# Performance work log

Hardware: AMD Instinct MI355X
Metric: run time of the kernel (lower is better)

The kernel has to match this reference:

```python
import jax, jax.numpy as jnp
import numpy as np

N = 50000       # nodes
F_IN = 256
F_OUT = 64
H = 4           # heads
DEG = 16        # avg degree (random edges per node)
NEG_SLOPE = 0.2


def setup_inputs() -> dict:
    key = jax.random.key(0)
    k_h, k_e, k_w, k_fc = jax.random.split(key, 4)
    h = jax.random.normal(k_h, (N, F_IN), dtype=jnp.float32)
    # random edges + explicit self-loops so every node has >= 1 out-edge
    e_rand = jax.random.randint(k_e, (2, N * DEG), 0, N, dtype=jnp.int64)
    loops = jnp.tile(jnp.arange(N, dtype=jnp.int64)[None, :], (2, 1))
    edge_index = jnp.concatenate([e_rand, loops], axis=1)  # [2, 850000]
    # Glorot-uniform-like scales
    s_w = np.sqrt(6.0 / (F_IN + F_OUT)).astype(np.float32)
    s_a = np.sqrt(6.0 / (2 * F_OUT + 1)).astype(np.float32)
    w = jax.random.uniform(k_w, (H, F_IN, F_OUT), jnp.float32, -s_w, s_w)
    fc = jax.random.uniform(k_fc, (H, 2 * F_OUT, 1), jnp.float32, -s_a, s_a)
    bias = jnp.zeros((F_OUT,), jnp.float32)
    return {"h": h, "edge_index": edge_index, "w": w, "fc": fc, "bias": bias}


def reference(h, edge_index, w, fc, bias):
    # GAT forward, vectorized over edges (dropout is identity at inference).
    n = h.shape[0]
    f_out = w.shape[2]
    src, dst = edge_index[0], edge_index[1]           # [E]
    h_prime = jnp.einsum('nf,hfo->hno', h, w)          # [H, N, F]
    a = fc[..., 0]                                     # [H, 2F]
    a_src, a_dst = a[:, :f_out], a[:, f_out:]          # [H, F] each
    s_src = jnp.einsum('hnf,hf->hn', h_prime, a_src)   # [H, N] score of center node
    s_dst = jnp.einsum('hnf,hf->hn', h_prime, a_dst)   # [H, N] score of neighbor
    e = jax.nn.leaky_relu(s_src[:, src] + s_dst[:, dst], NEG_SLOPE)  # [H, E]
    e = e.T                                            # [E, H]
    # segment softmax over edges grouped by source node
    seg_max = jax.ops.segment_max(e, src, num_segments=n)   # [N, H]
    ex = jnp.exp(e - seg_max[src])                           # [E, H]
    denom = jax.ops.segment_sum(ex, src, num_segments=n)    # [N, H]
    alpha = ex / denom[src]                                  # [E, H]
    # scatter-aggregate: out_i = sum_{j in N(i)} alpha_ij * Wh_j
    msgs = alpha[:, :, None] * jnp.transpose(h_prime[:, dst, :], (1, 0, 2))  # [E, H, F]
    out = jax.ops.segment_sum(msgs, src, num_segments=n)    # [N, H, F]
    return out.mean(axis=1) + bias                           # [N, F]
```

## Files before the change

### kernel.cpp

```cpp
#include <hip/hip_runtime.h>
#include <cfloat>

#define FIN 256
#define FOUT 64
#define NH 4
#define NEG_SLOPE 0.2f
#define SLOTS 64
#define BCAP 3072
#define P1T 4096

typedef __bf16 bf16x8 __attribute__((ext_vector_type(8)));
typedef float f32x4 __attribute__((ext_vector_type(4)));

__device__ __forceinline__ ushort f2bf(float f) {
    return (ushort)((__float_as_uint(f) + 0x8000u) >> 16);
}
__device__ __forceinline__ float bf2f(ushort u) {
    return __uint_as_float(((unsigned)u) << 16);
}
__device__ __forceinline__ float lrelu(float x) {
    return (x >= 0.f) ? x : NEG_SLOPE * x;
}

__global__ __launch_bounds__(256) void k0_wconv(const float* __restrict__ w,
                                                ushort* __restrict__ wt,
                                                int* __restrict__ gcur, int gn)
{
    if ((int)blockIdx.x < 256) {
        const int g = blockIdx.x * 256 + threadIdx.x;
        const int hh  = g >> 14;
        const int rem = g & 16383;
        const int c   = rem >> 8;
        const int k   = rem & 255;
        wt[g] = f2bf(w[(((hh << 8) | k) << 6) | c]);
    } else {
        const int g = ((int)blockIdx.x - 256) * 256 + threadIdx.x;
        if (g < gn) gcur[g] = 0;
    }
}

__global__ __launch_bounds__(256) void k1a(
    const int* __restrict__ ei, int E, int nbuck,
    int* __restrict__ gcur, unsigned* __restrict__ barea)
{
    __shared__ int lcnt[512];
    __shared__ int lscan[512];
    __shared__ int lbase[512];
    __shared__ unsigned ledges[P1T];
    const int tid = threadIdx.x;

    for (int b = tid; b < 512; b += 256) lcnt[b] = 0;
    __syncthreads();

    const int e0 = (int)blockIdx.x * P1T;
    const int cnt_total = min(P1T, E - e0);
    int s[16], d[16];
#pragma unroll
    for (int i = 0; i < 16; ++i) {
        const int e = e0 + i * 256 + tid;
        if (e < E) {
            s[i] = ei[e];
            d[i] = ei[E + e];
            atomicAdd(&lcnt[s[i] >> 7], 1);
        } else {
            s[i] = -1; d[i] = 0;
        }
    }
    __syncthreads();

    if (tid < 64) {
        int vals[8], sum = 0;
#pragma unroll
        for (int k = 0; k < 8; ++k) { vals[k] = lcnt[tid * 8 + k]; sum += vals[k]; }
        int x = sum;
#pragma unroll
        for (int dd = 1; dd < 64; dd <<= 1) {
            const int t = __shfl_up(x, dd);
            if (tid >= dd) x += t;
        }
        int run = x - sum;
#pragma unroll
        for (int k = 0; k < 8; ++k) { lscan[tid * 8 + k] = run; run += vals[k]; }
    }
    __syncthreads();

    for (int b = tid; b < nbuck; b += 256) {
        const int c = lcnt[b];
        lbase[b] = c ? atomicAdd(&gcur[b * 16], c) : 0;
    }
    __syncthreads();
    for (int b = tid; b < 512; b += 256) lcnt[b] = 0;
    __syncthreads();

#pragma unroll
    for (int i = 0; i < 16; ++i) {
        if (s[i] >= 0) {
            const int b = s[i] >> 7;
            const int r = atomicAdd(&lcnt[b], 1);
            ledges[lscan[b] + r] =
                ((unsigned)b << 23) | ((unsigned)(s[i] & 127) << 16) |
                (unsigned)d[i];
        }
    }
    __syncthreads();

    for (int j = tid; j < cnt_total; j += 256) {
        const unsigned p = ledges[j];
        const int b = (int)(p >> 23);
        const int pos = lbase[b] + (j - lscan[b]);
        if (pos < BCAP)
            barea[(size_t)b * BCAP + pos] = p & 0x007FFFFFu;
    }
}

#define ASTRIDE 280
#define OSTRIDE 260
__global__ __launch_bounds__(512) void k_gemm(
    const float* __restrict__ h, const ushort* __restrict__ wt,
    const float* __restrict__ fc, ushort* __restrict__ hp,
    float* __restrict__ s_src, float* __restrict__ s_dst, int N)
{
    __shared__ ushort lds[64 * ASTRIDE];
    const int tid = threadIdx.x;
    const int n0 = (int)blockIdx.x * 64;

    {
        float4 va[8];
#pragma unroll
        for (int i = 0; i < 8; ++i) {
            const int idx = i * 512 + tid;
            const int row  = idx >> 6;
            const int quad = idx & 63;
            const int n = n0 + row;
            va[i] = (n < N) ? ((const float4*)(h + (size_t)n * FIN))[quad]
                            : make_float4(0.f, 0.f, 0.f, 0.f);
        }
#pragma unroll
        for (int i = 0; i < 8; ++i) {
            const int idx = i * 512 + tid;
            const int row  = idx >> 6;
            const int quad = idx & 63;
            ushort4 bv;
            bv.x = f2bf(va[i].x); bv.y = f2bf(va[i].y);
            bv.z = f2bf(va[i].z); bv.w = f2bf(va[i].w);
            *(ushort4*)&lds[row * ASTRIDE + quad * 4] = bv;
        }
    }
    __syncthreads();

    const int wid   = tid >> 6;
    const int head  = wid & 3;
    const int mhalf = wid >> 2;
    const int lane  = tid & 63;
    const int lrow  = lane & 15;
    const int lq    = lane >> 4;

    const ushort* wth = wt + head * (64 * 256);

    f32x4 acc[2][4];
#pragma unroll
    for (int mt = 0; mt < 2; ++mt)
#pragma unroll
        for (int nt = 0; nt < 4; ++nt)
            acc[mt][nt] = (f32x4){0.f, 0.f, 0.f, 0.f};

#pragma unroll
    for (int kt = 0; kt < 8; ++kt) {
        const int kof = kt * 32 + lq * 8;
        bf16x8 bfr[4];
#pragma unroll
        for (int nt = 0; nt < 4; ++nt)
            bfr[nt] = *(const bf16x8*)&wth[(nt * 16 + lrow) * 256 + kof];
        bf16x8 af[2];
#pragma unroll
        for (int mt = 0; mt < 2; ++mt)
            af[mt] = *(const bf16x8*)
                &lds[(mhalf * 32 + mt * 16 + lrow) * ASTRIDE + kof];
#pragma unroll
        for (int nt = 0; nt < 4; ++nt)
#pragma unroll
            for (int mt = 0; mt < 2; ++mt)
                acc[mt][nt] = __builtin_amdgcn_mfma_f32_16x16x32_bf16(
                    af[mt], bfr[nt], acc[mt][nt], 0, 0, 0);
    }

    float as_[4], ad_[4];
#pragma unroll
    for (int nt = 0; nt < 4; ++nt) {
        as_[nt] = fc[head * 2 * FOUT + nt * 16 + lrow];
        ad_[nt] = fc[head * 2 * FOUT + FOUT + nt * 16 + lrow];
    }
#pragma unroll
    for (int mt = 0; mt < 2; ++mt) {
        const int rbase = n0 + mhalf * 32 + mt * 16 + lq * 4;
#pragma unroll
        for (int r = 0; r < 4; ++r) {
            const int n = rbase + r;
            float ps = 0.f, pd = 0.f;
#pragma unroll
            for (int nt = 0; nt < 4; ++nt) {
                const float v = acc[mt][nt][r];
                ps = fmaf(v, as_[nt], ps);
                pd = fmaf(v, ad_[nt], pd);
            }
            ps += __shfl_xor(ps, 1); pd += __shfl_xor(pd, 1);
            ps += __shfl_xor(ps, 2); pd += __shfl_xor(pd, 2);
            ps += __shfl_xor(ps, 4); pd += __shfl_xor(pd, 4);
            ps += __shfl_xor(ps, 8); pd += __shfl_xor(pd, 8);
            if (lrow == 0 && n < N) {
                s_src[(size_t)n * NH + head] = ps;
                s_dst[(size_t)n * NH + head] = pd;
            }
        }
    }

    __syncthreads();
#pragma unroll
    for (int mt = 0; mt < 2; ++mt)
#pragma unroll
        for (int r = 0; r < 4; ++r)
#pragma unroll
            for (int nt = 0; nt < 4; ++nt)
                lds[(mhalf * 32 + mt * 16 + lq * 4 + r) * OSTRIDE +
                    (nt * 16 + lrow) * 4 + head] = f2bf(acc[mt][nt][r]);
    __syncthreads();
    for (int idx = tid; idx < 64 * 64; idx += 512) {
        const int row = idx >> 6;
        const int c   = idx & 63;
        const int n = n0 + row;
        if (n < N)
            *(ushort4*)&hp[(size_t)n * 256 + c * 4] =
                *(const ushort4*)&lds[row * OSTRIDE + c * 4];
    }
}

__global__ __launch_bounds__(256) void k2(
    const int* __restrict__ gcur, const unsigned* __restrict__ barea,
    ushort* __restrict__ col, int* __restrict__ cursor)
{
    __shared__ ushort colT[128 * SLOTS];
    __shared__ int cnt[128];
    const int tid = threadIdx.x;
    const int b = blockIdx.x;
    for (int i = tid; i < 128; i += 256) cnt[i] = 0;
    __syncthreads();
    int c = gcur[b * 16];
    if (c > BCAP) c = BCAP;
    for (int j = tid; j < c; j += 256) {
        const unsigned p = barea[(size_t)b * BCAP + j];
        const int sl = (int)((p >> 16) & 127);
        const int r = atomicAdd(&cnt[sl], 1);
        if (r < SLOTS) colT[sl * SLOTS + r] = (ushort)(p & 0xFFFFu);
    }
    __syncthreads();
    const size_t gbase = (size_t)b * 128 * SLOTS;
    for (int idx = tid; idx < 128 * SLOTS / 4; idx += 256)
        *(ushort4*)&col[gbase + (size_t)idx * 4] =
            *(const ushort4*)&colT[idx * 4];
    for (int i = tid; i < 128; i += 256)
        cursor[b * 128 + i] = cnt[i];
}

__global__ __launch_bounds__(256) void k_agg(
    const int* __restrict__ cursor, const ushort* __restrict__ col,
    const ushort* __restrict__ hp,
    const float* __restrict__ s_src, const float* __restrict__ s_dst,
    const float* __restrict__ bias, float* __restrict__ out, int N)
{
    const int wid  = threadIdx.x >> 6;
    const int lane = threadIdx.x & 63;
    const int n    = blockIdx.x * 4 + wid;
    if (n >= N) return;

    const size_t start = (size_t)n * SLOTS;
    const int deg = min(cursor[n], SLOTS);
    const float4 ssn = ((const float4*)s_src)[n];
    const float4* sd4 = (const float4*)s_dst;

    float4 acc = make_float4(0.f, 0.f, 0.f, 0.f);

    int dreg = 0;
    float4 x = make_float4(-FLT_MAX, -FLT_MAX, -FLT_MAX, -FLT_MAX);
    if (lane < deg) {
        dreg = col[start + lane];
        const float4 sd = sd4[dreg];
        x.x = lrelu(ssn.x + sd.x);
        x.y = lrelu(ssn.y + sd.y);
        x.z = lrelu(ssn.z + sd.z);
        x.w = lrelu(ssn.w + sd.w);
    }
    float4 m = x;
#pragma unroll
    for (int d = 32; d; d >>= 1) {
        m.x = fmaxf(m.x, __shfl_xor(m.x, d));
        m.y = fmaxf(m.y, __shfl_xor(m.y, d));
        m.z = fmaxf(m.z, __shfl_xor(m.z, d));
        m.w = fmaxf(m.w, __shfl_xor(m.w, d));
    }
    float4 e = make_float4(0.f, 0.f, 0.f, 0.f);
    if (lane < deg) {
        e.x = __expf(x.x - m.x);
        e.y = __expf(x.y - m.y);
        e.z = __expf(x.z - m.z);
        e.w = __expf(x.w - m.w);
    }
    float4 s = e;
#pragma unroll
    for (int d = 32; d; d >>= 1) {
        s.x += __shfl_xor(s.x, d);
        s.y += __shfl_xor(s.y, d);
        s.z += __shfl_xor(s.z, d);
        s.w += __shfl_xor(s.w, d);
    }
    float4 alpha;
    alpha.x = e.x / s.x;
    alpha.y = e.y / s.y;
    alpha.z = e.z / s.z;
    alpha.w = e.w / s.w;

    const int nblk = (deg + 3) >> 2;
    for (int b = 0; b < nblk; ++b) {
        int dd[4]; float4 av[4]; ushort4 v[4];
#pragma unroll
        for (int u = 0; u < 4; ++u) {
            const int j = b * 4 + u;
            dd[u]   = __shfl(dreg, j);
            av[u].x = __shfl(alpha.x, j);
            av[u].y = __shfl(alpha.y, j);
            av[u].z = __shfl(alpha.z, j);
            av[u].w = __shfl(alpha.w, j);
        }
#pragma unroll
        for (int u = 0; u < 4; ++u)
            v[u] = *(const ushort4*)&hp[((size_t)dd[u] * FOUT + lane) * NH];
#pragma unroll
        for (int u = 0; u < 4; ++u) {
            acc.x = fmaf(av[u].x, bf2f(v[u].x), acc.x);
            acc.y = fmaf(av[u].y, bf2f(v[u].y), acc.y);
            acc.z = fmaf(av[u].z, bf2f(v[u].z), acc.z);
            acc.w = fmaf(av[u].w, bf2f(v[u].w), acc.w);
        }
    }

    out[(size_t)n * FOUT + lane] =
        (acc.x + acc.y + acc.z + acc.w) * 0.25f + bias[lane];
}

extern "C" void kernel_launch(void* const* d_in, const int* in_sizes, int n_in,
                              void* d_out, int out_size, void* d_ws, size_t ws_size,
                              hipStream_t stream)
{
    const float* h    = (const float*)d_in[0];
    const int*   ei   = (const int*)d_in[1];
    const float* w    = (const float*)d_in[2];
    const float* fc   = (const float*)d_in[3];
    const float* bias = (const float*)d_in[4];
    float* out = (float*)d_out;

    const int N = in_sizes[0] / FIN;
    const int E = in_sizes[1] / 2;
    const int nbuck = (N + 127) >> 7;

    char* ws = (char*)d_ws;
    auto take = [&](size_t bytes) {
        char* p = ws;
        ws += (bytes + 255) & ~(size_t)255;
        return p;
    };
    ushort*   wt      = (ushort*)take((size_t)NH * FIN * FOUT * sizeof(ushort));
    ushort*   h_prime = (ushort*)take((size_t)NH * N * FOUT * sizeof(ushort));
    float*    s_src   = (float*)take((size_t)NH * N * sizeof(float));
    float*    s_dst   = (float*)take((size_t)NH * N * sizeof(float));
    int*      cursor  = (int*)take((size_t)nbuck * 128 * sizeof(int));
    ushort*   col     = (ushort*)take((size_t)nbuck * 128 * SLOTS * sizeof(ushort));
    int*      gcur    = (int*)take((size_t)nbuck * 16 * sizeof(int));
    unsigned* barea   = (unsigned*)take((size_t)nbuck * BCAP * sizeof(unsigned));

    const int gn = nbuck * 16;
    k0_wconv<<<256 + (gn + 255) / 256, 256, 0, stream>>>(w, wt, gcur, gn);

    const int p1B = (E + P1T - 1) / P1T;
    k1a<<<p1B, 256, 0, stream>>>(ei, E, nbuck, gcur, barea);

    k_gemm<<<(N + 63) / 64, 512, 0, stream>>>(h, wt, fc, h_prime,
                                              s_src, s_dst, N);

    k2<<<nbuck, 256, 0, stream>>>(gcur, barea, col, cursor);

    k_agg<<<(N + 3) / 4, 256, 0, stream>>>(cursor, col, h_prime,
                                           s_src, s_dst, bias, out, N);
}
```

Measured before the change: 151.6 us.

## Pre-convert h to bf16 in edge-bucketing kernel and split aggregation launch

The fp32-to-bf16 conversion of h moves out of the GEMM and into extra blocks of the edge-bucketing kernel, so the GEMM loads half the bytes per tile and skips the conversion step. The aim is to overlap the memory-bound conversion with the edge-partitioning work. This adds a full extra read of h in fp32 plus a bf16 write and reread through a new workspace buffer. The aggregation kernel is also split into three launches over node ranges, which adds launch overhead with no clear benefit on a single stream.

```diff
diff --git a/kernel.cpp b/kernel.cpp
--- a/kernel.cpp
+++ b/kernel.cpp
@@ -11,6 +11,7 @@
 
 typedef __bf16 bf16x8 __attribute__((ext_vector_type(8)));
 typedef float f32x4 __attribute__((ext_vector_type(4)));
+typedef unsigned short ushort8 __attribute__((ext_vector_type(8)));
 
 __device__ __forceinline__ ushort f2bf(float f) {
     return (ushort)((__float_as_uint(f) + 0x8000u) >> 16);
@@ -39,15 +40,35 @@
     }
 }
 
-__global__ __launch_bounds__(256) void k1a(
+__global__ __launch_bounds__(256) void k_prep(
     const int* __restrict__ ei, int E, int nbuck,
-    int* __restrict__ gcur, unsigned* __restrict__ barea)
+    int* __restrict__ gcur, unsigned* __restrict__ barea, int p1B,
+    const float* __restrict__ h, ushort* __restrict__ hbf, int hElems)
 {
     __shared__ int lcnt[512];
     __shared__ int lscan[512];
     __shared__ int lbase[512];
     __shared__ unsigned ledges[P1T];
     const int tid = threadIdx.x;
+
+    if ((int)blockIdx.x >= p1B) {
+        const int t = ((int)blockIdx.x - p1B) * 256 + tid;
+        const size_t base = (size_t)t * 16;
+        if (base + 16 <= (size_t)hElems) {
+            const float4* h4 = (const float4*)(h + base);
+            const float4 a0 = h4[0], a1 = h4[1], a2 = h4[2], a3 = h4[3];
+            ushort8 b0, b1;
+            b0[0]=f2bf(a0.x); b0[1]=f2bf(a0.y); b0[2]=f2bf(a0.z); b0[3]=f2bf(a0.w);
+            b0[4]=f2bf(a1.x); b0[5]=f2bf(a1.y); b0[6]=f2bf(a1.z); b0[7]=f2bf(a1.w);
+            b1[0]=f2bf(a2.x); b1[1]=f2bf(a2.y); b1[2]=f2bf(a2.z); b1[3]=f2bf(a2.w);
+            b1[4]=f2bf(a3.x); b1[5]=f2bf(a3.y); b1[6]=f2bf(a3.z); b1[7]=f2bf(a3.w);
+            *(ushort8*)&hbf[base]     = b0;
+            *(ushort8*)&hbf[base + 8] = b1;
+        } else {
+            for (size_t i = base; i < (size_t)hElems; ++i) hbf[i] = f2bf(h[i]);
+        }
+        return;
+    }
 
     for (int b = tid; b < 512; b += 256) lcnt[b] = 0;
     __syncthreads();
@@ -115,8 +136,8 @@
 
 #define ASTRIDE 280
 #define OSTRIDE 260
-__global__ __launch_bounds__(512) void k_gemm(
-    const float* __restrict__ h, const ushort* __restrict__ wt,
+__global__ __launch_bounds__(512) void k_gemmB(
+    const ushort* __restrict__ hbf, const ushort* __restrict__ wt,
     const float* __restrict__ fc, ushort* __restrict__ hp,
     float* __restrict__ s_src, float* __restrict__ s_dst, int N)
 {
@@ -125,25 +146,23 @@
     const int n0 = (int)blockIdx.x * 64;
 
     {
-        float4 va[8];
-#pragma unroll
-        for (int i = 0; i < 8; ++i) {
+        ushort8 va[4];
+#pragma unroll
+        for (int i = 0; i < 4; ++i) {
             const int idx = i * 512 + tid;
-            const int row  = idx >> 6;
-            const int quad = idx & 63;
+            const int row = idx >> 5;
+            const int ch  = idx & 31;
             const int n = n0 + row;
-            va[i] = (n < N) ? ((const float4*)(h + (size_t)n * FIN))[quad]
-                            : make_float4(0.f, 0.f, 0.f, 0.f);
-        }
-#pragma unroll
-        for (int i = 0; i < 8; ++i) {
+            ushort8 v = (ushort8)0;
+            if (n < N) v = *(const ushort8*)&hbf[(size_t)n * FIN + ch * 8];
+            va[i] = v;
+        }
+#pragma unroll
+        for (int i = 0; i < 4; ++i) {
             const int idx = i * 512 + tid;
-            const int row  = idx >> 6;
-            const int quad = idx & 63;
-            ushort4 bv;
-            bv.x = f2bf(va[i].x); bv.y = f2bf(va[i].y);
-            bv.z = f2bf(va[i].z); bv.w = f2bf(va[i].w);
-            *(ushort4*)&lds[row * ASTRIDE + quad * 4] = bv;
+            const int row = idx >> 5;
+            const int ch  = idx & 31;
+            *(ushort8*)&lds[row * ASTRIDE + ch * 8] = va[i];
         }
     }
     __syncthreads();
@@ -265,11 +284,11 @@
     const int* __restrict__ cursor, const ushort* __restrict__ col,
     const ushort* __restrict__ hp,
     const float* __restrict__ s_src, const float* __restrict__ s_dst,
-    const float* __restrict__ bias, float* __restrict__ out, int N)
+    const float* __restrict__ bias, float* __restrict__ out, int N, int base)
 {
     const int wid  = threadIdx.x >> 6;
     const int lane = threadIdx.x & 63;
-    const int n    = blockIdx.x * 4 + wid;
+    const int n    = base + blockIdx.x * 4 + wid;
     if (n >= N) return;
 
     const size_t start = (size_t)n * SLOTS;
@@ -360,6 +379,7 @@
     const int N = in_sizes[0] / FIN;
     const int E = in_sizes[1] / 2;
     const int nbuck = (N + 127) >> 7;
+    const int hElems = N * FIN;
 
     char* ws = (char*)d_ws;
     auto take = [&](size_t bytes) {
@@ -369,6 +389,7 @@
     };
     ushort*   wt      = (ushort*)take((size_t)NH * FIN * FOUT * sizeof(ushort));
     ushort*   h_prime = (ushort*)take((size_t)NH * N * FOUT * sizeof(ushort));
+    ushort*   hbf     = (ushort*)take((size_t)hElems * sizeof(ushort));
     float*    s_src   = (float*)take((size_t)NH * N * sizeof(float));
     float*    s_dst   = (float*)take((size_t)NH * N * sizeof(float));
     int*      cursor  = (int*)take((size_t)nbuck * 128 * sizeof(int));
@@ -379,14 +400,23 @@
     const int gn = nbuck * 16;
     k0_wconv<<<256 + (gn + 255) / 256, 256, 0, stream>>>(w, wt, gcur, gn);
 
-    const int p1B = (E + P1T - 1) / P1T;
-    k1a<<<p1B, 256, 0, stream>>>(ei, E, nbuck, gcur, barea);
-
-    k_gemm<<<(N + 63) / 64, 512, 0, stream>>>(h, wt, fc, h_prime,
-                                              s_src, s_dst, N);
+    const int p1B  = (E + P1T - 1) / P1T;
+    const int h2bB = (hElems / 16 + 255) / 256;
+    k_prep<<<p1B + h2bB, 256, 0, stream>>>(ei, E, nbuck, gcur, barea, p1B,
+                                           h, hbf, hElems);
+
+    k_gemmB<<<(N + 63) / 64, 512, 0, stream>>>(hbf, wt, fc, h_prime,
+                                               s_src, s_dst, N);
 
     k2<<<nbuck, 256, 0, stream>>>(gcur, barea, col, cursor);
 
-    k_agg<<<(N + 3) / 4, 256, 0, stream>>>(cursor, col, h_prime,
-                                           s_src, s_dst, bias, out, N);
-}
+    const int total_blocks = (N + 3) / 4;
+    const int tb = (total_blocks + 2) / 3;
+    k_agg<<<tb, 256, 0, stream>>>(cursor, col, h_prime, s_src, s_dst,
+                                  bias, out, N, 0);
+    k_agg<<<tb, 256, 0, stream>>>(cursor, col, h_prime, s_src, s_dst,
+                                  bias, out, N, tb * 4);
+    k_agg<<<total_blocks - 2 * tb, 256, 0, stream>>>(cursor, col, h_prime,
+                                                     s_src, s_dst, bias, out,
+                                                     N, 2 * tb * 4);
+}
```

After: 168.7 us. +11.3%, slower.
